# Kernel optimization log

Measured on AMD Instinct MI355X. Metric: run time of the kernel, lower is better.

The kernel has to match this reference:

```python
import jax, jax.numpy as jnp
import numpy as np

TREE_DEPTH = 6
IN_F, OUT_F = 1024, 1024
BATCH = 2048
N_LEAVES = 2 ** TREE_DEPTH
N_NODES = N_LEAVES - 1


def _tree_routes(depth):
    """Static routing table: for each leaf, the decision-node index visited at
    each depth and whether the leaf takes the sigmoid (1) or 1-sigmoid (0) branch.
    Mirrors the torch traversal: node = 2*node + 1 + bit; bits of leaf id LSB-first."""
    n_leaves = 2 ** depth
    idx = np.zeros((n_leaves, depth), dtype=np.int32)
    pos = np.zeros((n_leaves, depth), dtype=bool)
    for l in range(n_leaves):
        node, index = 0, l
        for d in range(depth):
            idx[l, d] = node
            pos[l, d] = (index % 2 == 0)
            node = node * 2 + 1 + index % 2
            index >>= 1
    return idx, pos

ROUTE_IDX, ROUTE_POS = _tree_routes(TREE_DEPTH)


def setup_inputs() -> dict:
    key = jax.random.key(0)
    kx, kwd, kwl = jax.random.split(key, 3)
    scale = 0.02  # keep sigmoid/softmax logits in a sane range
    x = jax.random.normal(kx, (BATCH, IN_F), dtype=jnp.float32)
    Wd = jax.random.normal(kwd, (N_NODES, IN_F), dtype=jnp.float32) * scale
    bd = jnp.zeros((N_NODES,), dtype=jnp.float32)
    Wl = jax.random.normal(kwl, (N_LEAVES, OUT_F, IN_F), dtype=jnp.float32) * scale
    bl = jnp.zeros((N_LEAVES, OUT_F), dtype=jnp.float32)
    return {"x": x, "Wd": Wd, "bd": bd, "Wl": Wl, "bl": bl}


def reference(x, Wd, bd, Wl, bl):
    # All decision node probabilities in one GEMM: [B, n_nodes]
    dprob = jax.nn.sigmoid(x @ Wd.T + bd)
    # Gather per-leaf path probs [B, L, depth] and take path product -> routing [B, L]
    path = dprob[:, ROUTE_IDX]                      # [B, L, D]
    path = jnp.where(ROUTE_POS, path, 1.0 - path)
    routing = jnp.prod(path, axis=-1)               # [B, L]
    # All leaf experts in one batched GEMM: [B, L, out], softmax over out (torch dim=1)
    leaf_logits = jnp.einsum('bi,loi->blo', x, Wl) + bl
    leaves = jax.nn.softmax(leaf_logits, axis=-1)
    # Routing-weighted sum over leaves
    return jnp.einsum('bl,blo->bo', routing, leaves)
```

## Files before the change

kernel.cpp:

```cpp
#include <hip/hip_runtime.h>
#include <hip/hip_bf16.h>

#define BATCH 2048
#define KD 1024
#define ND 1024
#define NLEAF 64
#define BM 256
#define BN 128

typedef __attribute__((ext_vector_type(8))) short bf16x8;
typedef __attribute__((ext_vector_type(4))) float f32x4;
typedef __attribute__((ext_vector_type(8))) _Float16 f16x8;

#define WLB_OFF 0ULL
#define XB_OFF  134217728ULL
#define RT_OFF  138412032ULL
#define LG_OFF  138936320ULL

__device__ __forceinline__ unsigned short f2bf(float f) {
  unsigned int u = __float_as_uint(f);
  u += 0x7fffu + ((u >> 16) & 1u);
  return (unsigned short)(u >> 16);
}

__device__ __forceinline__ void gload_lds16(const void* g, void* l) {
  __builtin_amdgcn_global_load_lds(
      (const __attribute__((address_space(1))) unsigned int*)g,
      (__attribute__((address_space(3))) unsigned int*)l, 16, 0, 0);
}

__global__ void __launch_bounds__(256) convert_kernel(
    const float* __restrict__ Wl, const float* __restrict__ x,
    unsigned short* __restrict__ wlb, unsigned short* __restrict__ xb) {
  const long long WL4 = 16777216LL;
  const long long X4  = 524288LL;
  long long i = (long long)blockIdx.x * 256 + threadIdx.x;
  const long long stride = (long long)gridDim.x * 256;
  for (; i < WL4 + X4; i += stride) {
    float4 v;
    if (i < WL4) v = ((const float4*)Wl)[i];
    else         v = ((const float4*)x)[i - WL4];
    ushort4 o;
    o.x = f2bf(v.x); o.y = f2bf(v.y); o.z = f2bf(v.z); o.w = f2bf(v.w);
    if (i < WL4) ((ushort4*)wlb)[i] = o;
    else         ((ushort4*)xb)[i - WL4] = o;
  }
}

__global__ void __launch_bounds__(256) routing_kernel(
    const float* __restrict__ x, const float* __restrict__ Wd,
    const float* __restrict__ bd, float* __restrict__ rt) {
  __shared__ float xs[4][KD];
  __shared__ float sdp[4][64];
  const int tid = threadIdx.x;
  const int b0 = blockIdx.x * 4;
  const float4* xsrc = (const float4*)(x + (size_t)b0 * KD);
  float4* xdst = (float4*)&xs[0][0];
  for (int i = tid; i < KD; i += 256) xdst[i] = xsrc[i];
  __syncthreads();
  const int wv = tid >> 6, ln = tid & 63;
  const int b = b0 + wv;
  if (ln < 63) {
    const float4* wrow = (const float4*)(Wd + (size_t)ln * KD);
    const float4* xr = (const float4*)&xs[wv][0];
    float4 a = {0.f, 0.f, 0.f, 0.f};
    for (int k = 0; k < KD / 4; ++k) {
      float4 w = wrow[k], xv = xr[k];
      a.x += w.x * xv.x; a.y += w.y * xv.y; a.z += w.z * xv.z; a.w += w.w * xv.w;
    }
    float z = a.x + a.y + a.z + a.w + bd[ln];
    sdp[wv][ln] = 1.f / (1.f + __expf(-z));
  }
  __syncthreads();
  float prod = 1.f;
  int node = 0, index = ln;
  for (int d = 0; d < 6; ++d) {
    float pv = sdp[wv][node];
    prod *= (index & 1) ? (1.f - pv) : pv;
    node = node * 2 + 1 + (index & 1);
    index >>= 1;
  }
  rt[(size_t)b * NLEAF + ln] = prod;
}

__global__ void __launch_bounds__(512, 4) gemm_kernel(
    const unsigned short* __restrict__ A, const unsigned short* __restrict__ B,
    const float* __restrict__ blg, _Float16* __restrict__ C, int ntile) {
  extern __shared__ char smem[];
  const int tid = threadIdx.x;
  const int w = tid >> 6, ln = tid & 63;
  const int wm = w >> 1, wn = w & 1;
  const int g = ln >> 4, r16 = ln & 15;
  const int bid = blockIdx.x;
  const int j = bid >> 3;
  const int bm = (j & 7) * BM;
  const int bn = (((j >> 3) << 3) + (bid & 7)) * BN;
  const long long ldc = (long long)ntile * BN;

  const int rS = tid >> 2;
  const int cS = tid & 3;
  const int csrc = cS ^ ((rS >> 1) & 3);
  const unsigned short* ga0 = A + (size_t)(bm + rS) * KD + csrc * 8;
  const unsigned short* ga1 = ga0 + (size_t)128 * KD;
  const unsigned short* gb0 = B + (size_t)(bn + rS) * KD + csrc * 8;
  const int ldsw = w * 1024;

  auto STAGE = [&](int t) {
    char* base = smem + (t % 3) * 24576;
    const size_t ko = (size_t)t * 32;
    gload_lds16(ga0 + ko, base + ldsw);
    gload_lds16(ga1 + ko, base + 8192 + ldsw);
    gload_lds16(gb0 + ko, base + 16384 + ldsw);
  };

  int offA[4], offB[4];
#pragma unroll
  for (int mi = 0; mi < 4; ++mi) {
    const int row = wm * 64 + mi * 16 + r16;
    offA[mi] = row * 64 + (g ^ ((row >> 1) & 3)) * 16;
  }
#pragma unroll
  for (int ni = 0; ni < 4; ++ni) {
    const int row = wn * 64 + ni * 16 + r16;
    offB[ni] = 16384 + row * 64 + (g ^ ((row >> 1) & 3)) * 16;
  }

  f32x4 acc[4][4];
#pragma unroll
  for (int mi = 0; mi < 4; ++mi)
#pragma unroll
    for (int ni = 0; ni < 4; ++ni) acc[mi][ni] = (f32x4){0.f, 0.f, 0.f, 0.f};

  STAGE(0); STAGE(1);
  asm volatile("s_waitcnt vmcnt(3)" ::: "memory");
  asm volatile("s_barrier" ::: "memory");

  for (int t = 0; t < 32; ++t) {
    const char* buf = smem + (t % 3) * 24576;
    bf16x8 af[4], bf[4];
#pragma unroll
    for (int mi = 0; mi < 4; ++mi) af[mi] = *(const bf16x8*)(buf + offA[mi]);
#pragma unroll
    for (int ni = 0; ni < 4; ++ni) bf[ni] = *(const bf16x8*)(buf + offB[ni]);
    asm volatile("s_waitcnt lgkmcnt(0)" ::: "memory");
    __builtin_amdgcn_sched_barrier(0);
    if (t + 2 < 32) STAGE(t + 2);
    if (t < 30) asm volatile("s_waitcnt vmcnt(3)" ::: "memory");
    else        asm volatile("s_waitcnt vmcnt(0)" ::: "memory");
    asm volatile("s_barrier" ::: "memory");
    __builtin_amdgcn_s_setprio(1);
#pragma unroll
    for (int mi = 0; mi < 4; ++mi)
#pragma unroll
      for (int ni = 0; ni < 4; ++ni)
        acc[mi][ni] = __builtin_amdgcn_mfma_f32_16x16x32_bf16(
            af[mi], bf[ni], acc[mi][ni], 0, 0, 0);
    __builtin_amdgcn_s_setprio(0);
    __builtin_amdgcn_sched_barrier(0);
  }

  const int lf = bn >> 10;
  float blv[4];
#pragma unroll
  for (int ni = 0; ni < 4; ++ni)
    blv[ni] = blg[(size_t)lf * ND + (bn & 1023) + wn * 64 + ni * 16 + r16];
#pragma unroll
  for (int mi = 0; mi < 4; ++mi)
#pragma unroll
    for (int q = 0; q < 4; ++q) {
      const long long grow = bm + wm * 64 + mi * 16 + g * 4 + q;
#pragma unroll
      for (int ni = 0; ni < 4; ++ni) {
        const int gcol = bn + wn * 64 + ni * 16 + r16;
        C[grow * ldc + gcol] = (_Float16)(acc[mi][ni][q] + blv[ni]);
      }
    }
}

__global__ void __launch_bounds__(256) smax_kernel(
    const _Float16* __restrict__ Cg, const float* __restrict__ rt,
    float* __restrict__ out, int lpg, int l0, int first) {
  const int tid = threadIdx.x;
  const int wv = tid >> 6, ln = tid & 63;
  const int b = blockIdx.x * 4 + wv;
  const long long ldc = (long long)lpg * ND;
  const _Float16* base = Cg + (size_t)b * ldc + ln * 8;
  const float rtv = (ln < lpg) ? rt[(size_t)b * NLEAF + l0 + ln] : 0.f;

  float oacc[16];
#pragma unroll
  for (int k = 0; k < 16; ++k) oacc[k] = 0.f;

  for (int jj = 0; jj < lpg; ++jj) {
    const f16x8 h0 = *(const f16x8*)(base + jj * ND);
    const f16x8 h1 = *(const f16x8*)(base + jj * ND + 512);
    float e[16], s = 0.f;
#pragma unroll
    for (int k = 0; k < 8; ++k) { e[k] = __expf((float)h0[k]); s += e[k]; }
#pragma unroll
    for (int k = 0; k < 8; ++k) { e[8 + k] = __expf((float)h1[k]); s += e[8 + k]; }
#pragma unroll
    for (int off = 1; off < 64; off <<= 1) s += __shfl_xor(s, off);
    const float coef = __shfl(rtv, jj) / s;
#pragma unroll
    for (int k = 0; k < 16; ++k) oacc[k] += coef * e[k];
  }

  float* o0 = out + (size_t)b * ND + ln * 8;
  if (first) {
    *(float4*)o0         = (float4){oacc[0], oacc[1], oacc[2], oacc[3]};
    *(float4*)(o0 + 4)   = (float4){oacc[4], oacc[5], oacc[6], oacc[7]};
    *(float4*)(o0 + 512) = (float4){oacc[8], oacc[9], oacc[10], oacc[11]};
    *(float4*)(o0 + 516) = (float4){oacc[12], oacc[13], oacc[14], oacc[15]};
  } else {
#pragma unroll
    for (int part = 0; part < 4; ++part) {
      float* p = o0 + (part >> 1) * 512 + (part & 1) * 4;
      float4 v = *(const float4*)p;
      v.x += oacc[part * 4 + 0]; v.y += oacc[part * 4 + 1];
      v.z += oacc[part * 4 + 2]; v.w += oacc[part * 4 + 3];
      *(float4*)p = v;
    }
  }
}

extern "C" void kernel_launch(void* const* d_in, const int* in_sizes, int n_in,
                              void* d_out, int out_size, void* d_ws, size_t ws_size,
                              hipStream_t stream) {
  const float* x  = (const float*)d_in[0];
  const float* Wd = (const float*)d_in[1];
  const float* bd = (const float*)d_in[2];
  const float* Wl = (const float*)d_in[3];
  const float* bl = (const float*)d_in[4];
  float* out = (float*)d_out;
  char* ws = (char*)d_ws;
  unsigned short* wlb = (unsigned short*)(ws + WLB_OFF);
  unsigned short* xb  = (unsigned short*)(ws + XB_OFF);
  float* rt           = (float*)(ws + RT_OFF);
  _Float16* lg        = (_Float16*)(ws + LG_OFF);

  convert_kernel<<<2048, 256, 0, stream>>>(Wl, x, wlb, xb);
  routing_kernel<<<BATCH / 4, 256, 0, stream>>>(x, Wd, bd, rt);
  hipFuncSetAttribute((const void*)gemm_kernel,
                      hipFuncAttributeMaxDynamicSharedMemorySize, 73728);

  const int ngrp = (ws_size >= LG_OFF + (size_t)BATCH * NLEAF * ND * 2) ? 1 : 4;
  const int lpg = NLEAF / ngrp;
  const int ntile = lpg * (ND / BN);
  for (int grp = 0; grp < ngrp; ++grp) {
    gemm_kernel<<<8 * ntile, 512, 73728, stream>>>(
        xb, wlb + (size_t)grp * lpg * ND * KD,
        bl + (size_t)grp * lpg * ND, lg, ntile);
    smax_kernel<<<BATCH / 4, 256, 0, stream>>>(lg, rt, out,
                                               lpg, grp * lpg, grp == 0);
  }
}
```

Baseline: 505.0 us.

## Enlarge GEMM tile to 256x256 with 8-phase ping-pong K-pipeline

```diff
diff --git a/kernel.cpp b/kernel.cpp
--- a/kernel.cpp
+++ b/kernel.cpp
@@ -6,7 +6,7 @@
 #define ND 1024
 #define NLEAF 64
 #define BM 256
-#define BN 128
+#define BN 256
 
 typedef __attribute__((ext_vector_type(8))) short bf16x8;
 typedef __attribute__((ext_vector_type(4))) float f32x4;
@@ -83,80 +83,128 @@
   rt[(size_t)b * NLEAF + ln] = prod;
 }
 
-__global__ void __launch_bounds__(512, 4) gemm_kernel(
+#define BARR  asm volatile("s_barrier" ::: "memory")
+#define LGKM0 asm volatile("s_waitcnt lgkmcnt(0)" ::: "memory")
+#define VMC2  asm volatile("s_waitcnt vmcnt(2)" ::: "memory")
+#define VMC0  asm volatile("s_waitcnt vmcnt(0)" ::: "memory")
+#define SB0   __builtin_amdgcn_sched_barrier(0)
+#define PRIO1 __builtin_amdgcn_s_setprio(1)
+#define PRIO0 __builtin_amdgcn_s_setprio(0)
+
+#define RD_A(BUF, OFS)                                                       \
+  _Pragma("unroll") for (int mi = 0; mi < 4; ++mi) {                         \
+    aQ[mi][0] = *(const bf16x8*)((BUF) + offA[(OFS) + mi]);                  \
+    aQ[mi][1] = *(const bf16x8*)((BUF) + (offA[(OFS) + mi] ^ 64));           \
+  }
+#define RD_B(DST, BUF, OFS)                                                  \
+  _Pragma("unroll") for (int nj = 0; nj < 2; ++nj) {                         \
+    DST[nj][0] = *(const bf16x8*)((BUF) + offB[(OFS) + nj]);                 \
+    DST[nj][1] = *(const bf16x8*)((BUF) + (offB[(OFS) + nj] ^ 64));          \
+  }
+#define MFMA_Q(H, J, BR)                                                     \
+  PRIO1;                                                                     \
+  _Pragma("unroll") for (int mi = 0; mi < 4; ++mi)                           \
+  _Pragma("unroll") for (int nj = 0; nj < 2; ++nj) {                         \
+    acc[4*(H)+mi][2*(J)+nj] = __builtin_amdgcn_mfma_f32_16x16x32_bf16(       \
+        aQ[mi][0], BR[nj][0], acc[4*(H)+mi][2*(J)+nj], 0, 0, 0);             \
+    acc[4*(H)+mi][2*(J)+nj] = __builtin_amdgcn_mfma_f32_16x16x32_bf16(       \
+        aQ[mi][1], BR[nj][1], acc[4*(H)+mi][2*(J)+nj], 0, 0, 0);             \
+  }                                                                          \
+  PRIO0; SB0
+
+__global__ void __launch_bounds__(512, 2) gemm_kernel(
     const unsigned short* __restrict__ A, const unsigned short* __restrict__ B,
     const float* __restrict__ blg, _Float16* __restrict__ C, int ntile) {
   extern __shared__ char smem[];
   const int tid = threadIdx.x;
   const int w = tid >> 6, ln = tid & 63;
-  const int wm = w >> 1, wn = w & 1;
+  const int wm = w >> 2, wn = w & 3;
   const int g = ln >> 4, r16 = ln & 15;
   const int bid = blockIdx.x;
   const int j = bid >> 3;
   const int bm = (j & 7) * BM;
   const int bn = (((j >> 3) << 3) + (bid & 7)) * BN;
-  const long long ldc = (long long)ntile * BN;
-
-  const int rS = tid >> 2;
-  const int cS = tid & 3;
-  const int csrc = cS ^ ((rS >> 1) & 3);
-  const unsigned short* ga0 = A + (size_t)(bm + rS) * KD + csrc * 8;
-  const unsigned short* ga1 = ga0 + (size_t)128 * KD;
-  const unsigned short* gb0 = B + (size_t)(bn + rS) * KD + csrc * 8;
+  const long long ldc = (long long)ntile * 256;
+
+  const int sr = tid >> 3, sj = tid & 7;
+  const int sjx = sj ^ (sr & 7);
+  const unsigned short* gA = A + (size_t)(bm + sr) * KD + (size_t)sjx * 8;
+  const unsigned short* gB = B + (size_t)(bn + sr) * KD + (size_t)sjx * 8;
   const int ldsw = w * 1024;
 
-  auto STAGE = [&](int t) {
-    char* base = smem + (t % 3) * 24576;
-    const size_t ko = (size_t)t * 32;
-    gload_lds16(ga0 + ko, base + ldsw);
-    gload_lds16(ga1 + ko, base + 8192 + ldsw);
-    gload_lds16(gb0 + ko, base + 16384 + ldsw);
+  auto STAGE_H = [&](int t, int which) {
+    char* dst = smem + ((t & 1) << 16) + which * 16384 + ldsw;
+    const unsigned short* s = ((which < 2) ? gA : gB) +
+        (((size_t)(which & 1)) << 7) * KD + ((size_t)t << 6);
+    gload_lds16(s, dst);
+    gload_lds16(s + (size_t)64 * KD, dst + 8192);
   };
 
-  int offA[4], offB[4];
-#pragma unroll
-  for (int mi = 0; mi < 4; ++mi) {
-    const int row = wm * 64 + mi * 16 + r16;
-    offA[mi] = row * 64 + (g ^ ((row >> 1) & 3)) * 16;
-  }
-#pragma unroll
-  for (int ni = 0; ni < 4; ++ni) {
-    const int row = wn * 64 + ni * 16 + r16;
-    offB[ni] = 16384 + row * 64 + (g ^ ((row >> 1) & 3)) * 16;
-  }
-
-  f32x4 acc[4][4];
-#pragma unroll
-  for (int mi = 0; mi < 4; ++mi)
+  const int swz = (g ^ (r16 & 7)) * 16;
+  int offA[8], offB[4];
+#pragma unroll
+  for (int mi = 0; mi < 8; ++mi)
+    offA[mi] = wm * 16384 + (mi * 16 + r16) * 128 + swz;
+#pragma unroll
+  for (int ni = 0; ni < 4; ++ni)
+    offB[ni] = (2 + (wn >> 1)) * 16384 + ((wn & 1) * 64 + ni * 16 + r16) * 128 + swz;
+
+  f32x4 acc[8][4];
+#pragma unroll
+  for (int mi = 0; mi < 8; ++mi)
 #pragma unroll
     for (int ni = 0; ni < 4; ++ni) acc[mi][ni] = (f32x4){0.f, 0.f, 0.f, 0.f};
 
-  STAGE(0); STAGE(1);
-  asm volatile("s_waitcnt vmcnt(3)" ::: "memory");
-  asm volatile("s_barrier" ::: "memory");
-
-  for (int t = 0; t < 32; ++t) {
-    const char* buf = smem + (t % 3) * 24576;
-    bf16x8 af[4], bf[4];
-#pragma unroll
-    for (int mi = 0; mi < 4; ++mi) af[mi] = *(const bf16x8*)(buf + offA[mi]);
-#pragma unroll
-    for (int ni = 0; ni < 4; ++ni) bf[ni] = *(const bf16x8*)(buf + offB[ni]);
-    asm volatile("s_waitcnt lgkmcnt(0)" ::: "memory");
-    __builtin_amdgcn_sched_barrier(0);
-    if (t + 2 < 32) STAGE(t + 2);
-    if (t < 30) asm volatile("s_waitcnt vmcnt(3)" ::: "memory");
-    else        asm volatile("s_waitcnt vmcnt(0)" ::: "memory");
-    asm volatile("s_barrier" ::: "memory");
-    __builtin_amdgcn_s_setprio(1);
-#pragma unroll
-    for (int mi = 0; mi < 4; ++mi)
-#pragma unroll
-      for (int ni = 0; ni < 4; ++ni)
-        acc[mi][ni] = __builtin_amdgcn_mfma_f32_16x16x32_bf16(
-            af[mi], bf[ni], acc[mi][ni], 0, 0, 0);
-    __builtin_amdgcn_s_setprio(0);
-    __builtin_amdgcn_sched_barrier(0);
+  const char* b0 = smem;
+  const char* b1 = smem + 65536;
+  bf16x8 aQ[4][2], b01[2][2], b23[2][2];
+
+  STAGE_H(0, 0); STAGE_H(0, 1); STAGE_H(0, 2); STAGE_H(0, 3);
+  STAGE_H(1, 0);
+  VMC2; BARR;
+
+  for (int i = 0; i < 8; ++i) {
+    const int t0 = 2 * i, t1 = 2 * i + 1;
+    const bool pf = (i < 7);
+    RD_A(b0, 0); RD_B(b01, b0, 0);
+    STAGE_H(t1, 1);
+    BARR; LGKM0; SB0;
+    MFMA_Q(0, 0, b01);
+    BARR;
+    RD_B(b23, b0, 2);
+    STAGE_H(t1, 2);
+    BARR; LGKM0; SB0;
+    MFMA_Q(0, 1, b23);
+    BARR;
+    RD_A(b0, 4);
+    STAGE_H(t1, 3);
+    BARR; LGKM0; SB0;
+    MFMA_Q(1, 0, b01);
+    BARR;
+    if (pf) { STAGE_H(t0 + 2, 0); VMC2; } else { VMC0; }
+    BARR;
+    MFMA_Q(1, 1, b23);
+    BARR;
+    RD_A(b1, 0); RD_B(b01, b1, 0);
+    if (pf) STAGE_H(t0 + 2, 1);
+    BARR; LGKM0; SB0;
+    MFMA_Q(0, 0, b01);
+    BARR;
+    RD_B(b23, b1, 2);
+    if (pf) STAGE_H(t0 + 2, 2);
+    BARR; LGKM0; SB0;
+    MFMA_Q(0, 1, b23);
+    BARR;
+    RD_A(b1, 4);
+    if (pf) STAGE_H(t0 + 2, 3);
+    BARR; LGKM0; SB0;
+    MFMA_Q(1, 0, b01);
+    BARR;
+    if (pf) STAGE_H(t0 + 3, 0);
+    VMC2;
+    BARR;
+    MFMA_Q(1, 1, b23);
+    if (pf) BARR;
   }
 
   const int lf = bn >> 10;
@@ -165,10 +213,10 @@
   for (int ni = 0; ni < 4; ++ni)
     blv[ni] = blg[(size_t)lf * ND + (bn & 1023) + wn * 64 + ni * 16 + r16];
 #pragma unroll
-  for (int mi = 0; mi < 4; ++mi)
+  for (int mi = 0; mi < 8; ++mi)
 #pragma unroll
     for (int q = 0; q < 4; ++q) {
-      const long long grow = bm + wm * 64 + mi * 16 + g * 4 + q;
+      const long long grow = bm + wm * 128 + mi * 16 + g * 4 + q;
 #pragma unroll
       for (int ni = 0; ni < 4; ++ni) {
         const int gcol = bn + wn * 64 + ni * 16 + r16;
@@ -242,13 +290,13 @@
   convert_kernel<<<2048, 256, 0, stream>>>(Wl, x, wlb, xb);
   routing_kernel<<<BATCH / 4, 256, 0, stream>>>(x, Wd, bd, rt);
   hipFuncSetAttribute((const void*)gemm_kernel,
-                      hipFuncAttributeMaxDynamicSharedMemorySize, 73728);
+                      hipFuncAttributeMaxDynamicSharedMemorySize, 131072);
 
   const int ngrp = (ws_size >= LG_OFF + (size_t)BATCH * NLEAF * ND * 2) ? 1 : 4;
   const int lpg = NLEAF / ngrp;
   const int ntile = lpg * (ND / BN);
   for (int grp = 0; grp < ngrp; ++grp) {
-    gemm_kernel<<<8 * ntile, 512, 73728, stream>>>(
+    gemm_kernel<<<8 * ntile, 512, 131072, stream>>>(
         xb, wlb + (size_t)grp * lpg * ND * KD,
         bl + (size_t)grp * lpg * ND, lg, ntile);
     smax_kernel<<<BATCH / 4, 256, 0, stream>>>(lg, rt, out,
```

New measurement: 524.4 us. 1.04x slower.

## Enlarge leaf GEMM tile to 256x256 with 64-wide K double-buffered staging

Applied to the files above, without the earlier changes.

```diff
diff --git a/kernel.cpp b/kernel.cpp
--- a/kernel.cpp
+++ b/kernel.cpp
@@ -5,8 +5,10 @@
 #define KD 1024
 #define ND 1024
 #define NLEAF 64
+#define NGRP 2
+#define LPG 32
 #define BM 256
-#define BN 128
+#define BN 256
 
 typedef __attribute__((ext_vector_type(8))) short bf16x8;
 typedef __attribute__((ext_vector_type(4))) float f32x4;
@@ -83,80 +85,86 @@
   rt[(size_t)b * NLEAF + ln] = prod;
 }
 
-__global__ void __launch_bounds__(512, 4) gemm_kernel(
+__global__ void __launch_bounds__(512, 2) gemm_kernel(
     const unsigned short* __restrict__ A, const unsigned short* __restrict__ B,
     const float* __restrict__ blg, _Float16* __restrict__ C, int ntile) {
   extern __shared__ char smem[];
   const int tid = threadIdx.x;
   const int w = tid >> 6, ln = tid & 63;
-  const int wm = w >> 1, wn = w & 1;
+  const int wm = w >> 2, wn = w & 3;
   const int g = ln >> 4, r16 = ln & 15;
   const int bid = blockIdx.x;
   const int j = bid >> 3;
   const int bm = (j & 7) * BM;
   const int bn = (((j >> 3) << 3) + (bid & 7)) * BN;
-  const long long ldc = (long long)ntile * BN;
-
-  const int rS = tid >> 2;
-  const int cS = tid & 3;
-  const int csrc = cS ^ ((rS >> 1) & 3);
-  const unsigned short* ga0 = A + (size_t)(bm + rS) * KD + csrc * 8;
-  const unsigned short* ga1 = ga0 + (size_t)128 * KD;
-  const unsigned short* gb0 = B + (size_t)(bn + rS) * KD + csrc * 8;
+  const long long ldc = (long long)ntile * 256;
+
+  const int sr = tid >> 3, sj = tid & 7;
+  const int sjx = sj ^ (sr & 7);
+  const unsigned short* gA = A + (size_t)(bm + sr) * KD + sjx * 8;
+  const unsigned short* gB = B + (size_t)(bn + sr) * KD + sjx * 8;
   const int ldsw = w * 1024;
 
   auto STAGE = [&](int t) {
-    char* base = smem + (t % 3) * 24576;
-    const size_t ko = (size_t)t * 32;
-    gload_lds16(ga0 + ko, base + ldsw);
-    gload_lds16(ga1 + ko, base + 8192 + ldsw);
-    gload_lds16(gb0 + ko, base + 16384 + ldsw);
+    char* base = smem + (t & 1) * 65536;
+    const size_t ko = (size_t)t * 64;
+#pragma unroll
+    for (int p = 0; p < 4; ++p) {
+      gload_lds16(gA + (size_t)(p * 64) * KD + ko, base + p * 8192 + ldsw);
+      gload_lds16(gB + (size_t)(p * 64) * KD + ko, base + 32768 + p * 8192 + ldsw);
+    }
   };
 
-  int offA[4], offB[4];
-#pragma unroll
-  for (int mi = 0; mi < 4; ++mi) {
-    const int row = wm * 64 + mi * 16 + r16;
-    offA[mi] = row * 64 + (g ^ ((row >> 1) & 3)) * 16;
+  int offA[8], offB[4];
+#pragma unroll
+  for (int mi = 0; mi < 8; ++mi) {
+    const int row = wm * 128 + mi * 16 + r16;
+    offA[mi] = row * 128 + ((g ^ (row & 7)) * 16);
   }
 #pragma unroll
   for (int ni = 0; ni < 4; ++ni) {
     const int row = wn * 64 + ni * 16 + r16;
-    offB[ni] = 16384 + row * 64 + (g ^ ((row >> 1) & 3)) * 16;
-  }
-
-  f32x4 acc[4][4];
-#pragma unroll
-  for (int mi = 0; mi < 4; ++mi)
+    offB[ni] = 32768 + row * 128 + ((g ^ (row & 7)) * 16);
+  }
+
+  f32x4 acc[8][4];
+#pragma unroll
+  for (int mi = 0; mi < 8; ++mi)
 #pragma unroll
     for (int ni = 0; ni < 4; ++ni) acc[mi][ni] = (f32x4){0.f, 0.f, 0.f, 0.f};
 
-  STAGE(0); STAGE(1);
-  asm volatile("s_waitcnt vmcnt(3)" ::: "memory");
-  asm volatile("s_barrier" ::: "memory");
-
-  for (int t = 0; t < 32; ++t) {
-    const char* buf = smem + (t % 3) * 24576;
-    bf16x8 af[4], bf[4];
-#pragma unroll
-    for (int mi = 0; mi < 4; ++mi) af[mi] = *(const bf16x8*)(buf + offA[mi]);
-#pragma unroll
-    for (int ni = 0; ni < 4; ++ni) bf[ni] = *(const bf16x8*)(buf + offB[ni]);
-    asm volatile("s_waitcnt lgkmcnt(0)" ::: "memory");
-    __builtin_amdgcn_sched_barrier(0);
-    if (t + 2 < 32) STAGE(t + 2);
-    if (t < 30) asm volatile("s_waitcnt vmcnt(3)" ::: "memory");
-    else        asm volatile("s_waitcnt vmcnt(0)" ::: "memory");
+  STAGE(0);
+
+  for (int t = 0; t < 16; ++t) {
+    asm volatile("s_waitcnt vmcnt(0)" ::: "memory");
     asm volatile("s_barrier" ::: "memory");
+    if (t + 1 < 16) STAGE(t + 1);
+    const char* buf = smem + (t & 1) * 65536;
+    bf16x8 a0[8], a1[8], b0r[4], b1r[4];
+#pragma unroll
+    for (int mi = 0; mi < 8; ++mi) {
+      a0[mi] = *(const bf16x8*)(buf + offA[mi]);
+      a1[mi] = *(const bf16x8*)(buf + (offA[mi] ^ 64));
+    }
+#pragma unroll
+    for (int ni = 0; ni < 4; ++ni) {
+      b0r[ni] = *(const bf16x8*)(buf + offB[ni]);
+      b1r[ni] = *(const bf16x8*)(buf + (offB[ni] ^ 64));
+    }
     __builtin_amdgcn_s_setprio(1);
 #pragma unroll
-    for (int mi = 0; mi < 4; ++mi)
+    for (int mi = 0; mi < 8; ++mi)
 #pragma unroll
       for (int ni = 0; ni < 4; ++ni)
         acc[mi][ni] = __builtin_amdgcn_mfma_f32_16x16x32_bf16(
-            af[mi], bf[ni], acc[mi][ni], 0, 0, 0);
+            a0[mi], b0r[ni], acc[mi][ni], 0, 0, 0);
+#pragma unroll
+    for (int mi = 0; mi < 8; ++mi)
+#pragma unroll
+      for (int ni = 0; ni < 4; ++ni)
+        acc[mi][ni] = __builtin_amdgcn_mfma_f32_16x16x32_bf16(
+            a1[mi], b1r[ni], acc[mi][ni], 0, 0, 0);
     __builtin_amdgcn_s_setprio(0);
-    __builtin_amdgcn_sched_barrier(0);
   }
 
   const int lf = bn >> 10;
@@ -165,10 +173,10 @@
   for (int ni = 0; ni < 4; ++ni)
     blv[ni] = blg[(size_t)lf * ND + (bn & 1023) + wn * 64 + ni * 16 + r16];
 #pragma unroll
-  for (int mi = 0; mi < 4; ++mi)
+  for (int mi = 0; mi < 8; ++mi)
 #pragma unroll
     for (int q = 0; q < 4; ++q) {
-      const long long grow = bm + wm * 64 + mi * 16 + g * 4 + q;
+      const long long grow = bm + wm * 128 + mi * 16 + g * 4 + q;
 #pragma unroll
       for (int ni = 0; ni < 4; ++ni) {
         const int gcol = bn + wn * 64 + ni * 16 + r16;
@@ -242,16 +250,14 @@
   convert_kernel<<<2048, 256, 0, stream>>>(Wl, x, wlb, xb);
   routing_kernel<<<BATCH / 4, 256, 0, stream>>>(x, Wd, bd, rt);
   hipFuncSetAttribute((const void*)gemm_kernel,
-                      hipFuncAttributeMaxDynamicSharedMemorySize, 73728);
-
-  const int ngrp = (ws_size >= LG_OFF + (size_t)BATCH * NLEAF * ND * 2) ? 1 : 4;
-  const int lpg = NLEAF / ngrp;
-  const int ntile = lpg * (ND / BN);
-  for (int grp = 0; grp < ngrp; ++grp) {
-    gemm_kernel<<<8 * ntile, 512, 73728, stream>>>(
-        xb, wlb + (size_t)grp * lpg * ND * KD,
-        bl + (size_t)grp * lpg * ND, lg, ntile);
+                      hipFuncAttributeMaxDynamicSharedMemorySize, 131072);
+
+  const int ntile = LPG * (ND / BN);
+  for (int grp = 0; grp < NGRP; ++grp) {
+    gemm_kernel<<<8 * ntile, 512, 131072, stream>>>(
+        xb, wlb + (size_t)grp * LPG * ND * KD,
+        bl + (size_t)grp * LPG * ND, lg, ntile);
     smax_kernel<<<BATCH / 4, 256, 0, stream>>>(lg, rt, out,
-                                               lpg, grp * lpg, grp == 0);
-  }
-}
+                                               LPG, grp * LPG, grp == 0);
+  }
+}
```

Measured after the change: 463.3 us, median of 4. 1.09x faster.
